# Kernel tuning notes

Hardware: AMD Instinct MI355X
Metric: run time of the kernel (lower is better)

The kernel has to match this reference:

```python
import jax, jax.numpy as jnp
import numpy as np

N, D_IN, D, E, B = 30000, 512, 512, 300000, 4096
N_RES, N_DNN = 2, 2
EPS = 1e-5


def _ln(x, g, b):
    mu = jnp.mean(x, axis=-1, keepdims=True)
    var = jnp.mean((x - mu) ** 2, axis=-1, keepdims=True)
    return (x - mu) * jax.lax.rsqrt(var + EPS) * g + b


def setup_inputs() -> dict:
    key = jax.random.key(0)
    ks = jax.random.split(key, 16)
    s = 1.0 / np.sqrt(D)
    inp = {
        "node_feat": jax.random.normal(ks[0], (N, D_IN), jnp.float32),
        "edge_hop0": jax.random.randint(ks[1], (2, E), 0, N, jnp.int32),
        "edge_hop1": jax.random.randint(ks[2], (2, E), 0, N, jnp.int32),
        "target_idx": jax.random.randint(ks[3], (B,), 0, N, jnp.int32),
        # node transform
        "Wt": jax.random.normal(ks[4], (D_IN, D), jnp.float32) / np.sqrt(D_IN),
        "bt": jnp.zeros((D,), jnp.float32),
        # GATConv (shared across both hops, one relation)
        "Wf": jax.random.normal(ks[5], (D, D), jnp.float32) * s,
        "bf": jnp.zeros((D,), jnp.float32),
        "w_att": jax.random.normal(ks[6], (2 * D,), jnp.float32) * s,
        "b_att": jnp.zeros((), jnp.float32),
        "gat_bias": jnp.zeros((D,), jnp.float32),
        # Res_DNN
        "Wp": jax.random.normal(ks[7], (D, D), jnp.float32) * s,
        "bp": jnp.zeros((D,), jnp.float32),
        "dnn_W": jax.random.normal(ks[8], (N_RES, N_DNN, D, D), jnp.float32) * s,
        "dnn_b": jnp.zeros((N_RES, N_DNN, D), jnp.float32),
        "dnn_g": jnp.ones((N_RES, N_DNN, D), jnp.float32),
        "dnn_beta": jnp.zeros((N_RES, N_DNN, D), jnp.float32),
        "res_g": jnp.ones((N_RES, D), jnp.float32),
        "res_beta": jnp.zeros((N_RES, D), jnp.float32),
        "Wc": jax.random.normal(ks[9], (D, 1), jnp.float32) * s,
        "bc": jnp.zeros((1,), jnp.float32),
    }
    return inp


def _gat(feat, edges, Wf, bf, w_att, b_att, gat_bias):
    # dst and src are the same node set / same features here
    h = feat @ Wf + bf                      # [N, D]
    di, si = edges[0], edges[1]             # [E], [E]
    # att(concat(dst_h, src_h)) == dst_h @ w[:D] + src_h @ w[D:] + b
    sd = h @ w_att[:D]                      # [N]
    ss = h @ w_att[D:]                      # [N]
    e = jnp.tanh(sd[di] + ss[si] + b_att)   # [E]
    # sparse softmax per destination row
    m = jax.ops.segment_max(e, di, num_segments=N)
    a = jnp.exp(e - m[di])
    denom = jax.ops.segment_sum(a, di, num_segments=N)
    alpha = a / denom[di]                   # [E]
    # sparse-mm aggregation
    out = jax.ops.segment_sum(alpha[:, None] * h[si], di, num_segments=N)
    return out + gat_bias


def reference(node_feat, edge_hop0, edge_hop1, target_idx, Wt, bt, Wf, bf,
              w_att, b_att, gat_bias, Wp, bp, dnn_W, dnn_b, dnn_g, dnn_beta,
              res_g, res_beta, Wc, bc):
    # node-type feature transform (dropout is identity at inference)
    feat = node_feat @ Wt + bt              # [N, D]
    # hops processed from last to first: hop1 then hop0
    for edges in (edge_hop1, edge_hop0):
        g = _gat(feat, edges, Wf, bf, w_att, b_att, gat_bias)
        feat = (feat + g) * 0.5             # mean of stacked [orig, gat_out]
    h = feat[target_idx]                    # [B, D]
    # Res_DNN head
    h = h @ Wp + bp
    for r in range(N_RES):
        sc = h
        for i in range(N_DNN):
            h = _ln(jnp.tanh(h @ dnn_W[r, i] + dnn_b[r, i]), dnn_g[r, i], dnn_beta[r, i])
        h = _ln(jnp.tanh(sc + h), res_g[r], res_beta[r])
    logits = h @ Wc + bc                    # [B, 1]
    return jax.nn.sigmoid(logits)
```

## Files before the change

### kernel.cpp

```cpp
#include <hip/hip_runtime.h>

#define D 512
typedef unsigned short ushort_t;
typedef __attribute__((ext_vector_type(8))) short bf16x8;
typedef __attribute__((ext_vector_type(4))) float f32x4;

static __device__ __forceinline__ ushort_t f2bf(float f) {
  unsigned u = __float_as_uint(f);
  u += 0x7fffu + ((u >> 16) & 1u);
  return (ushort_t)(u >> 16);
}
static __device__ __forceinline__ float bf2f(ushort_t h) {
  return __uint_as_float(((unsigned)h) << 16);
}

static __device__ __forceinline__ void gld_lds16(const void* g, void* lds) {
  __builtin_amdgcn_global_load_lds(
      (const __attribute__((address_space(1))) unsigned int*)g,
      (__attribute__((address_space(3))) unsigned int*)lds, 16, 0, 0);
}

__global__ __launch_bounds__(256) void pack_weight7(
    const float* __restrict__ Wt, const float* __restrict__ Wf,
    const float* __restrict__ Wp, const float* __restrict__ Wd,
    ushort_t* __restrict__ out) {
  const int per = D * D;
  int i = blockIdx.x * 256 + threadIdx.x;
  if (i >= per * 7) return;
  const int mat = i / per;
  const int r = i - mat * per;
  const float* W;
  if (mat == 0) W = Wt;
  else if (mat == 1) W = Wf;
  else if (mat == 2) W = Wp;
  else W = Wd + (size_t)(mat - 3) * per;
  const int k = r / D, n = r - k * D;
  const int nt = n >> 4, col = n & 15, kt = k >> 5, kg = (k >> 3) & 3, j = k & 7;
  out[(size_t)mat * per + (((size_t)nt * (D >> 5) + kt) << 9) + ((kg << 4) + col) * 8 + j] =
      f2bf(W[r]);
}

__global__ __launch_bounds__(256) void conv_bf16_pad(
    const float* __restrict__ in, ushort_t* __restrict__ out, int M, int Mp, int K) {
  const size_t i4 = ((size_t)blockIdx.x * 256 + threadIdx.x) * 4;
  if (i4 >= (size_t)Mp * K) return;
  const int row = (int)(i4 / K);
  ushort4 o;
  if (row < M) {
    const float4 v = *reinterpret_cast<const float4*>(&in[i4]);
    o.x = f2bf(v.x); o.y = f2bf(v.y); o.z = f2bf(v.z); o.w = f2bf(v.w);
  } else {
    o.x = o.y = o.z = o.w = 0;
  }
  *reinterpret_cast<ushort4*>(&out[i4]) = o;
}

__global__ __launch_bounds__(256) void init_buffers(
    int* __restrict__ cnt, int* __restrict__ tflag, int* __restrict__ nflag,
    int* __restrict__ counters, int Nn, int N2) {
  const int i = blockIdx.x * 256 + threadIdx.x;
  if (i < N2) cnt[i] = 0;
  if (i < Nn) { tflag[i] = 0; nflag[i] = 0; }
  if (i < 2) counters[i * 64] = 0;
}

__global__ void fill_bucket(const int* __restrict__ e1, const int* __restrict__ e0,
                            const int* __restrict__ tidx, int* __restrict__ tflag,
                            int* __restrict__ cnt, int* __restrict__ bucket,
                            int Nn, int E, int B) {
  const int e = blockIdx.x * blockDim.x + threadIdx.x;
  if (e < B) tflag[tidx[e]] = 1;
  if (e >= E) return;
  const int d1 = e1[e];
  const int p1 = atomicAdd(&cnt[d1], 1);
  if (p1 < 64) bucket[(size_t)d1 * 64 + p1] = e1[E + e];
  const int d0 = e0[e];
  const int p0 = atomicAdd(&cnt[Nn + d0], 1);
  if (p0 < 64) bucket[((size_t)(Nn + d0)) * 64 + p0] = e0[E + e];
}

__global__ void flag_srcs(const int* __restrict__ e0, const int* __restrict__ tflag,
                          int* __restrict__ nflag, int E) {
  const int e = blockIdx.x * blockDim.x + threadIdx.x;
  if (e < E && tflag[e0[e]]) nflag[e0[E + e]] = 1;
}

__global__ void compact2(const int* __restrict__ tflag, const int* __restrict__ nflag,
                         int* __restrict__ tlist, int* __restrict__ nlist,
                         int* __restrict__ counters, int Nn) {
  const int i = blockIdx.x * 256 + threadIdx.x;
  if (i >= Nn) return;
  const int tf = tflag[i];
  if (tf) tlist[atomicAdd(&counters[0], 1)] = i;
  if (tf | nflag[i]) nlist[atomicAdd(&counters[64], 1)] = i;
}

__global__ __launch_bounds__(512) void gemm_mfma(
    const ushort_t* __restrict__ A, const ushort_t* __restrict__ Bp,
    const float* __restrict__ bias, ushort_t* __restrict__ C16,
    const float* __restrict__ watt, float* __restrict__ sd_part,
    float* __restrict__ ss_part, int Mp, int N, int K) {
  __shared__ __align__(16) ushort_t As[2][8 * 512];
  __shared__ __align__(16) ushort_t Bs[2][8 * 512];
  const int nwg = gridDim.x;
  const int q = nwg >> 3, rm = nwg & 7;
  const int xcd = blockIdx.x & 7, kk = blockIdx.x >> 3;
  const int lin = (xcd < rm ? xcd * (q + 1) : rm * (q + 1) + (xcd - rm) * q) + kk;
  const int m0 = (lin >> 2) * 128;
  const int n0 = (lin & 3) * 128;
  const int tid = threadIdx.x;
  const int lane = tid & 63;
  const int wid = tid >> 6;
  const int wm = wid >> 1;
  const int wn = wid & 1;
  const int arow = lane & 15;
  const int akoff = (lane >> 4) * 8;
  const int c15 = lane & 15;
  const int rgrp = lane >> 4;
  const int kt32 = K >> 5;
  f32x4 acc[2][4] = {};

  auto stage = [&](int kt, int b) {
    const int k0 = kt * 32;
    gld_lds16(&A[(size_t)(m0 + wid * 16 + arow) * K + k0 + akoff],
              &As[b][wid * 512]);
    gld_lds16(&Bp[(((size_t)(n0 / 16 + wid) * kt32 + kt) << 9) + lane * 8],
              &Bs[b][wid * 512]);
  };

  stage(0, 0);
  __syncthreads();
  int cur = 0;
  for (int t = 0; t < kt32; ++t) {
    if (t + 1 < kt32) stage(t + 1, cur ^ 1);
    bf16x8 af[2], bfr[4];
#pragma unroll
    for (int mi = 0; mi < 2; ++mi)
      af[mi] = *reinterpret_cast<const bf16x8*>(&As[cur][(wm * 2 + mi) * 512 + lane * 8]);
#pragma unroll
    for (int ni = 0; ni < 4; ++ni)
      bfr[ni] = *reinterpret_cast<const bf16x8*>(&Bs[cur][(wn * 4 + ni) * 512 + lane * 8]);
#pragma unroll
    for (int mi = 0; mi < 2; ++mi)
#pragma unroll
      for (int ni = 0; ni < 4; ++ni)
        acc[mi][ni] = __builtin_amdgcn_mfma_f32_16x16x32_bf16(af[mi], bfr[ni], acc[mi][ni], 0, 0, 0);
    __syncthreads();
    cur ^= 1;
  }
  const int band = (n0 >> 6) + wn;
#pragma unroll
  for (int mi = 0; mi < 2; ++mi) {
    const int row = m0 + wm * 32 + mi * 16 + (rgrp << 2);
#pragma unroll
    for (int r = 0; r < 4; ++r) {
      float psd = 0.f, pss = 0.f;
#pragma unroll
      for (int ni = 0; ni < 4; ++ni) {
        const int col = n0 + wn * 64 + ni * 16 + c15;
        const float v = acc[mi][ni][r] + bias[col];
        C16[(size_t)(row + r) * N + col] = f2bf(v);
        if (watt) {
          psd += v * watt[col];
          pss += v * watt[D + col];
        }
      }
      if (watt) {
#pragma unroll
        for (int off = 8; off > 0; off >>= 1) {
          psd += __shfl_xor(psd, off);
          pss += __shfl_xor(pss, off);
        }
        if (c15 == 0) {
          sd_part[(size_t)band * Mp + row + r] = psd;
          ss_part[(size_t)band * Mp + row + r] = pss;
        }
      }
    }
  }
}

__global__ __launch_bounds__(256) void combine_dots(
    const float* __restrict__ sd_part, const float* __restrict__ ss_part,
    float* __restrict__ sd, float* __restrict__ ss, int Mp, int Nn) {
  const int i = blockIdx.x * 256 + threadIdx.x;
  if (i >= Nn) return;
  float a = 0.f, b = 0.f;
#pragma unroll
  for (int bnd = 0; bnd < 8; ++bnd) {
    a += sd_part[(size_t)bnd * Mp + i];
    b += ss_part[(size_t)bnd * Mp + i];
  }
  sd[i] = a;
  ss[i] = b;
}

__global__ __launch_bounds__(256) void gat_aggregate_w(
    ushort_t* __restrict__ featb, const ushort_t* __restrict__ hb,
    const float* __restrict__ sd, const float* __restrict__ ss,
    const int* __restrict__ di, const int* __restrict__ si,
    const float* __restrict__ b_att_p, const float* __restrict__ gat_bias,
    const int* __restrict__ cnt, const int* __restrict__ bucket,
    const int* __restrict__ dstlist, const int* __restrict__ dcount,
    int Nn, int E) {
  const int gidx = blockIdx.x * 4 + (threadIdx.x >> 6);
  const int lane = threadIdx.x & 63;
  if (gidx >= *dcount) return;
  const int dst = dstlist[gidx];
  const int deg = cnt[dst];
  const float sdd = sd[dst];
  const float ba = b_att_p[0];
  const size_t o = (size_t)dst * D + lane * 8;
  bf16x8 fv = *reinterpret_cast<const bf16x8*>(&featb[o]);
  float acc[8] = {};
  if (deg <= 64) {
    const bool valid = lane < deg;
    const int slane = valid ? bucket[(size_t)dst * 64 + lane] : 0;
    const float e = valid ? tanhf(sdd + ss[slane] + ba) : -1e30f;
    float m = e;
#pragma unroll
    for (int off = 32; off > 0; off >>= 1) m = fmaxf(m, __shfl_xor(m, off));
    const float a = valid ? expf(e - m) : 0.f;
    float s = a;
#pragma unroll
    for (int off = 32; off > 0; off >>= 1) s += __shfl_xor(s, off);
    const float w = a * ((s > 0.f) ? 1.f / s : 0.f);
    int k = 0;
    for (; k + 3 < deg; k += 4) {
      const float w0 = __shfl(w, k), w1 = __shfl(w, k + 1);
      const float w2 = __shfl(w, k + 2), w3 = __shfl(w, k + 3);
      const int s0 = __shfl(slane, k), s1 = __shfl(slane, k + 1);
      const int s2 = __shfl(slane, k + 2), s3 = __shfl(slane, k + 3);
      const bf16x8 h0 = *reinterpret_cast<const bf16x8*>(&hb[(size_t)s0 * D + lane * 8]);
      const bf16x8 h1 = *reinterpret_cast<const bf16x8*>(&hb[(size_t)s1 * D + lane * 8]);
      const bf16x8 h2 = *reinterpret_cast<const bf16x8*>(&hb[(size_t)s2 * D + lane * 8]);
      const bf16x8 h3 = *reinterpret_cast<const bf16x8*>(&hb[(size_t)s3 * D + lane * 8]);
#pragma unroll
      for (int qq = 0; qq < 8; ++qq) {
        const float t0 = w0 * bf2f((ushort_t)h0[qq]) + w1 * bf2f((ushort_t)h1[qq]);
        const float t1 = w2 * bf2f((ushort_t)h2[qq]) + w3 * bf2f((ushort_t)h3[qq]);
        acc[qq] += t0 + t1;
      }
    }
    for (; k < deg; ++k) {
      const float wk = __shfl(w, k);
      const int sk = __shfl(slane, k);
      const bf16x8 h0 = *reinterpret_cast<const bf16x8*>(&hb[(size_t)sk * D + lane * 8]);
#pragma unroll
      for (int qq = 0; qq < 8; ++qq) acc[qq] += wk * bf2f((ushort_t)h0[qq]);
    }
  } else {
    float m = -1e30f;
    for (int e = lane; e < E; e += 64)
      if (di[e] == dst) m = fmaxf(m, tanhf(sdd + ss[si[e]] + ba));
#pragma unroll
    for (int off = 32; off > 0; off >>= 1) m = fmaxf(m, __shfl_xor(m, off));
    float s = 0.f;
    for (int e = lane; e < E; e += 64)
      if (di[e] == dst) s += expf(tanhf(sdd + ss[si[e]] + ba) - m);
#pragma unroll
    for (int off = 32; off > 0; off >>= 1) s += __shfl_xor(s, off);
    const float inv = (s > 0.f) ? 1.f / s : 0.f;
    for (int base = 0; base < E; base += 64) {
      const int e = base + lane;
      const bool hit = (e < E) && (di[e] == dst);
      unsigned long long mask = __ballot(hit);
      const int sidx = hit ? si[e] : 0;
      const float aval = hit ? expf(tanhf(sdd + ss[sidx] + ba) - m) * inv : 0.f;
      while (mask) {
        const int l = __ffsll((long long)mask) - 1;
        mask &= mask - 1;
        const float wv = __shfl(aval, l);
        const int sk = __shfl(sidx, l);
        const bf16x8 hv = *reinterpret_cast<const bf16x8*>(&hb[(size_t)sk * D + lane * 8]);
#pragma unroll
        for (int qq = 0; qq < 8; ++qq) acc[qq] += wv * bf2f((ushort_t)hv[qq]);
      }
    }
  }
#pragma unroll
  for (int q = 0; q < 8; ++q) {
    const float f = (bf2f((ushort_t)fv[q]) + acc[q] + gat_bias[lane * 8 + q]) * 0.5f;
    fv[q] = (short)f2bf(f);
  }
  *reinterpret_cast<bf16x8*>(&featb[o]) = fv;
}

__global__ __launch_bounds__(1024, 4) void head_fused(
    const ushort_t* __restrict__ featb, const int* __restrict__ tidx,
    const ushort_t* __restrict__ pWp, const float* __restrict__ bp,
    const ushort_t* __restrict__ pDW, const float* __restrict__ dnn_b,
    const float* __restrict__ dnn_g, const float* __restrict__ dnn_be,
    const float* __restrict__ res_g, const float* __restrict__ res_be,
    const float* __restrict__ Wc, const float* __restrict__ bc,
    float* __restrict__ out) {
  __shared__ __align__(16) ushort_t A_lds[16 * 512];
  __shared__ float lsum[16][16], lsq[16][16], meanv[16], rsv[16];
  const int tid = threadIdx.x;
  const int lane = tid & 63;
  const int wave = tid >> 6;
  const int nt0 = wave * 2;
  const int c15 = lane & 15;
  const int rgrp = lane >> 4;

  {
    const int row = tid >> 6, col8 = tid & 63;
    const int g = tidx[blockIdx.x * 16 + row];
    const bf16x8 v = *reinterpret_cast<const bf16x8*>(&featb[(size_t)g * D + col8 * 8]);
    *reinterpret_cast<bf16x8*>(&A_lds[row * 512 + (col8 ^ (row & 7)) * 8]) = v;
  }
  __syncthreads();

  auto do_gemm = [&](const ushort_t* __restrict__ W, f32x4& a0, f32x4& a1) {
    a0 = f32x4{0.f, 0.f, 0.f, 0.f};
    a1 = f32x4{0.f, 0.f, 0.f, 0.f};
    bf16x8 c0[4], c1[4];
#pragma unroll
    for (int d = 0; d < 4; ++d) {
      c0[d] = *reinterpret_cast<const bf16x8*>(
          &W[(((size_t)nt0 * 16 + d) << 9) + lane * 8]);
      c1[d] = *reinterpret_cast<const bf16x8*>(
          &W[(((size_t)(nt0 + 1) * 16 + d) << 9) + lane * 8]);
    }
#pragma unroll
    for (int kt = 0; kt < 16; ++kt) {
      const int slot = kt & 3;
      const bf16x8 w0 = c0[slot];
      const bf16x8 w1 = c1[slot];
      if (kt + 4 < 16) {
        c0[slot] = *reinterpret_cast<const bf16x8*>(
            &W[(((size_t)nt0 * 16 + kt + 4) << 9) + lane * 8]);
        c1[slot] = *reinterpret_cast<const bf16x8*>(
            &W[(((size_t)(nt0 + 1) * 16 + kt + 4) << 9) + lane * 8]);
      }
      const int col8 = kt * 4 + rgrp;
      const bf16x8 af = *reinterpret_cast<const bf16x8*>(
          &A_lds[c15 * 512 + (col8 ^ (c15 & 7)) * 8]);
      a0 = __builtin_amdgcn_mfma_f32_16x16x32_bf16(af, w0, a0, 0, 0, 0);
      a1 = __builtin_amdgcn_mfma_f32_16x16x32_bf16(af, w1, a1, 0, 0, 0);
    }
  };

  auto block_ln = [&](f32x4& v0, f32x4& v1, const float* __restrict__ g,
                      const float* __restrict__ be) {
    float psum[4], psq[4];
#pragma unroll
    for (int r = 0; r < 4; ++r) {
      psum[r] = v0[r] + v1[r];
      psq[r] = v0[r] * v0[r] + v1[r] * v1[r];
    }
#pragma unroll
    for (int off = 8; off > 0; off >>= 1)
#pragma unroll
      for (int r = 0; r < 4; ++r) {
        psum[r] += __shfl_xor(psum[r], off);
        psq[r] += __shfl_xor(psq[r], off);
      }
    if (c15 == 0) {
#pragma unroll
      for (int r = 0; r < 4; ++r) {
        lsum[wave][rgrp * 4 + r] = psum[r];
        lsq[wave][rgrp * 4 + r] = psq[r];
      }
    }
    __syncthreads();
    if (tid < 16) {
      float s = 0.f, qq = 0.f;
#pragma unroll
      for (int w = 0; w < 16; ++w) { s += lsum[w][tid]; qq += lsq[w][tid]; }
      const float mean = s * (1.f / 512.f);
      const float var = qq * (1.f / 512.f) - mean * mean;
      meanv[tid] = mean;
      rsv[tid] = rsqrtf(var + 1e-5f);
    }
    __syncthreads();
    const int col0 = nt0 * 16 + c15;
    const int col1 = (nt0 + 1) * 16 + c15;
    const float g0 = g[col0], b0 = be[col0];
    const float g1 = g[col1], b1 = be[col1];
#pragma unroll
    for (int r = 0; r < 4; ++r) {
      const int row = rgrp * 4 + r;
      v0[r] = (v0[r] - meanv[row]) * rsv[row] * g0 + b0;
      v1[r] = (v1[r] - meanv[row]) * rsv[row] * g1 + b1;
    }
  };

  auto store_A = [&](const f32x4& v0, const f32x4& v1) {
    const int col0 = nt0 * 16 + c15;
    const int col1 = (nt0 + 1) * 16 + c15;
#pragma unroll
    for (int r = 0; r < 4; ++r) {
      const int row = rgrp * 4 + r;
      A_lds[row * 512 + (((col0 >> 3) ^ (row & 7)) << 3) + (col0 & 7)] = f2bf(v0[r]);
      A_lds[row * 512 + (((col1 >> 3) ^ (row & 7)) << 3) + (col1 & 7)] = f2bf(v1[r]);
    }
  };

  f32x4 sc0, sc1, acc0, acc1, ln0, ln1;

  do_gemm(pWp, acc0, acc1);
  {
    const float bv0 = bp[nt0 * 16 + c15];
    const float bv1 = bp[(nt0 + 1) * 16 + c15];
#pragma unroll
    for (int r = 0; r < 4; ++r) { sc0[r] = acc0[r] + bv0; sc1[r] = acc1[r] + bv1; }
  }
  __syncthreads();
  store_A(sc0, sc1);
  __syncthreads();

  for (int rb = 0; rb < 2; ++rb) {
    {
      const int st = rb * 2;
      do_gemm(pDW + (size_t)st * D * D, acc0, acc1);
      const float bv0 = dnn_b[st * D + nt0 * 16 + c15];
      const float bv1 = dnn_b[st * D + (nt0 + 1) * 16 + c15];
#pragma unroll
      for (int r = 0; r < 4; ++r) {
        acc0[r] = tanhf(acc0[r] + bv0);
        acc1[r] = tanhf(acc1[r] + bv1);
      }
      block_ln(acc0, acc1, dnn_g + st * D, dnn_be + st * D);
      store_A(acc0, acc1);
      __syncthreads();
    }
    {
      const int st = rb * 2 + 1;
      do_gemm(pDW + (size_t)st * D * D, ln0, ln1);
      const float bv0 = dnn_b[st * D + nt0 * 16 + c15];
      const float bv1 = dnn_b[st * D + (nt0 + 1) * 16 + c15];
#pragma unroll
      for (int r = 0; r < 4; ++r) {
        ln0[r] = tanhf(ln0[r] + bv0);
        ln1[r] = tanhf(ln1[r] + bv1);
      }
      block_ln(ln0, ln1, dnn_g + st * D, dnn_be + st * D);
    }
#pragma unroll
    for (int r = 0; r < 4; ++r) {
      acc0[r] = tanhf(sc0[r] + ln0[r]);
      acc1[r] = tanhf(sc1[r] + ln1[r]);
    }
    block_ln(acc0, acc1, res_g + rb * D, res_be + rb * D);
    sc0 = acc0;
    sc1 = acc1;
    if (rb == 0) {
      store_A(sc0, sc1);
      __syncthreads();
    }
  }

  float pr[4];
  {
    const float w0 = Wc[nt0 * 16 + c15];
    const float w1 = Wc[(nt0 + 1) * 16 + c15];
#pragma unroll
    for (int r = 0; r < 4; ++r) pr[r] = sc0[r] * w0 + sc1[r] * w1;
  }
#pragma unroll
  for (int off = 8; off > 0; off >>= 1)
#pragma unroll
    for (int r = 0; r < 4; ++r) pr[r] += __shfl_xor(pr[r], off);
  __syncthreads();
  if (c15 == 0) {
#pragma unroll
    for (int r = 0; r < 4; ++r) lsum[wave][rgrp * 4 + r] = pr[r];
  }
  __syncthreads();
  if (tid < 16) {
    float s = 0.f;
#pragma unroll
    for (int w = 0; w < 16; ++w) s += lsum[w][tid];
    out[blockIdx.x * 16 + tid] = 1.f / (1.f + expf(-(s + bc[0])));
  }
}

extern "C" void kernel_launch(void* const* d_in, const int* in_sizes, int n_in,
                              void* d_out, int out_size, void* d_ws, size_t ws_size,
                              hipStream_t stream) {
  (void)n_in; (void)out_size; (void)ws_size;
  const float* node_feat = (const float*)d_in[0];
  const int* edge0 = (const int*)d_in[1];
  const int* edge1 = (const int*)d_in[2];
  const int* tidx = (const int*)d_in[3];
  const float* Wt = (const float*)d_in[4];
  const float* bt = (const float*)d_in[5];
  const float* Wf = (const float*)d_in[6];
  const float* bfp = (const float*)d_in[7];
  const float* w_att = (const float*)d_in[8];
  const float* b_att = (const float*)d_in[9];
  const float* gat_bias = (const float*)d_in[10];
  const float* Wp = (const float*)d_in[11];
  const float* bp = (const float*)d_in[12];
  const float* dnn_W = (const float*)d_in[13];
  const float* dnn_b = (const float*)d_in[14];
  const float* dnn_g = (const float*)d_in[15];
  const float* dnn_be = (const float*)d_in[16];
  const float* res_g = (const float*)d_in[17];
  const float* res_be = (const float*)d_in[18];
  const float* Wc = (const float*)d_in[19];
  const float* bc = (const float*)d_in[20];
  float* out = (float*)d_out;

  const int Nn = in_sizes[0] / D;
  const int E = in_sizes[1] / 2;
  const int B = in_sizes[3];
  const int K_IN = in_sizes[4] / D;
  const int Mp = (Nn + 127) / 128 * 128;
  const int N2 = 2 * Nn;

  char* p = (char*)d_ws;
  auto alloc = [&](size_t bytes) -> char* {
    char* r = p;
    p += (bytes + 255) & ~(size_t)255;
    return r;
  };
  ushort_t* featb = (ushort_t*)alloc((size_t)Mp * D * 2);
  ushort_t* hb = (ushort_t*)alloc((size_t)Mp * D * 2);
  float* sd = (float*)alloc((size_t)Nn * 4);
  float* ss = (float*)alloc((size_t)Nn * 4);
  float* sd_part = (float*)alloc((size_t)8 * Mp * 4);
  float* ss_part = (float*)alloc((size_t)8 * Mp * 4);
  int* cnt = (int*)alloc((size_t)N2 * 4);
  int* bucket = (int*)alloc((size_t)N2 * 64 * 4);
  int* tflag = (int*)alloc((size_t)Nn * 4);
  int* nflag = (int*)alloc((size_t)Nn * 4);
  int* tlist = (int*)alloc((size_t)B * 4);
  int* nlist = (int*)alloc((size_t)Nn * 4);
  int* counters = (int*)alloc(512);
  ushort_t* pAll = (ushort_t*)alloc((size_t)7 * D * D * 2);
  ushort_t* pWt = pAll;
  ushort_t* pWf = pAll + (size_t)D * D;
  ushort_t* pWp = pAll + (size_t)2 * D * D;
  ushort_t* pDWall = pAll + (size_t)3 * D * D;

  dim3 blk(256);

  pack_weight7<<<(7 * D * D + 255) / 256, blk, 0, stream>>>(Wt, Wf, Wp, dnn_W, pAll);
  conv_bf16_pad<<<((size_t)Mp * K_IN / 4 + 255) / 256, blk, 0, stream>>>(
      node_feat, hb , Nn, Mp, K_IN);

  init_buffers<<<(N2 + 255) / 256, blk, 0, stream>>>(cnt, tflag, nflag, counters, Nn, N2);
  fill_bucket<<<(E + 255) / 256, blk, 0, stream>>>(edge1, edge0, tidx, tflag,
                                                   cnt, bucket, Nn, E, B);
  flag_srcs<<<(E + 255) / 256, blk, 0, stream>>>(edge0, tflag, nflag, E);
  compact2<<<(Nn + 255) / 256, blk, 0, stream>>>(tflag, nflag, tlist, nlist,
                                                 counters, Nn);

  gemm_mfma<<<dim3(4 * (Mp / 128)), dim3(512), 0, stream>>>(
      hb, pWt, bt, featb, nullptr, nullptr, nullptr, Mp, D, K_IN);

  const int* hops[2] = {edge1, edge0};
  for (int hp = 0; hp < 2; ++hp) {
    gemm_mfma<<<dim3(4 * (Mp / 128)), dim3(512), 0, stream>>>(
        featb, pWf, bfp, hb, w_att, sd_part, ss_part, Mp, D, D);
    combine_dots<<<(Nn + 255) / 256, blk, 0, stream>>>(sd_part, ss_part, sd, ss, Mp, Nn);
    if (hp == 0) {
      gat_aggregate_w<<<(Nn + 3) / 4, blk, 0, stream>>>(
          featb, hb, sd, ss, hops[hp], hops[hp] + E, b_att, gat_bias,
          cnt + hp * Nn, bucket + (size_t)hp * Nn * 64, nlist, &counters[64], Nn, E);
    } else {
      gat_aggregate_w<<<(B + 3) / 4, blk, 0, stream>>>(
          featb, hb, sd, ss, hops[hp], hops[hp] + E, b_att, gat_bias,
          cnt + hp * Nn, bucket + (size_t)hp * Nn * 64, tlist, &counters[0], Nn, E);
    }
  }

  head_fused<<<B / 16, dim3(1024), 0, stream>>>(
      featb, tidx, pWp, bp, pDWall, dnn_b, dnn_g, dnn_be, res_g, res_be,
      Wc, bc, out);
}
```

Measured before the change: 294.0 us.

## Shrink head_fused to 8 rows per block with 512 threads, 4 N-tiles per wave

The fused MLP head now handles 8 target rows per block instead of 16, using 8 waves that each own 4 output column tiles. Rows 8-15 of the 16-row MFMA operand are zero-padded, and the grid doubles to B/8 blocks. The explicit 4-deep register prefetch of weight fragments is removed in favour of direct loads inside the k loop. This spreads the head across more blocks to raise CU coverage, at the cost of half the MFMA work being spent on padding rows and each block re-reading the full weight matrices.

```diff
diff --git a/kernel.cpp b/kernel.cpp
--- a/kernel.cpp
+++ b/kernel.cpp
@@ -286,7 +286,7 @@
   *reinterpret_cast<bf16x8*>(&featb[o]) = fv;
 }
 
-__global__ __launch_bounds__(1024, 4) void head_fused(
+__global__ __launch_bounds__(512, 4) void head_fused(
     const ushort_t* __restrict__ featb, const int* __restrict__ tidx,
     const ushort_t* __restrict__ pWp, const float* __restrict__ bp,
     const ushort_t* __restrict__ pDW, const float* __restrict__ dnn_b,
@@ -295,60 +295,53 @@
     const float* __restrict__ Wc, const float* __restrict__ bc,
     float* __restrict__ out) {
   __shared__ __align__(16) ushort_t A_lds[16 * 512];
-  __shared__ float lsum[16][16], lsq[16][16], meanv[16], rsv[16];
+  __shared__ float lsum[8][8], lsq[8][8], meanv[8], rsv[8];
   const int tid = threadIdx.x;
   const int lane = tid & 63;
   const int wave = tid >> 6;
-  const int nt0 = wave * 2;
+  const int nt0 = wave * 4;
   const int c15 = lane & 15;
   const int rgrp = lane >> 4;
 
   {
     const int row = tid >> 6, col8 = tid & 63;
-    const int g = tidx[blockIdx.x * 16 + row];
+    const int g = tidx[blockIdx.x * 8 + row];
     const bf16x8 v = *reinterpret_cast<const bf16x8*>(&featb[(size_t)g * D + col8 * 8]);
     *reinterpret_cast<bf16x8*>(&A_lds[row * 512 + (col8 ^ (row & 7)) * 8]) = v;
+    const int rz = row + 8;
+    *reinterpret_cast<bf16x8*>(&A_lds[rz * 512 + (col8 ^ (rz & 7)) * 8]) = bf16x8{};
   }
   __syncthreads();
 
-  auto do_gemm = [&](const ushort_t* __restrict__ W, f32x4& a0, f32x4& a1) {
-    a0 = f32x4{0.f, 0.f, 0.f, 0.f};
-    a1 = f32x4{0.f, 0.f, 0.f, 0.f};
-    bf16x8 c0[4], c1[4];
-#pragma unroll
-    for (int d = 0; d < 4; ++d) {
-      c0[d] = *reinterpret_cast<const bf16x8*>(
-          &W[(((size_t)nt0 * 16 + d) << 9) + lane * 8]);
-      c1[d] = *reinterpret_cast<const bf16x8*>(
-          &W[(((size_t)(nt0 + 1) * 16 + d) << 9) + lane * 8]);
-    }
+  auto do_gemm = [&](const ushort_t* __restrict__ W, f32x4* a) {
+#pragma unroll
+    for (int ni = 0; ni < 4; ++ni) a[ni] = f32x4{0.f, 0.f, 0.f, 0.f};
 #pragma unroll
     for (int kt = 0; kt < 16; ++kt) {
-      const int slot = kt & 3;
-      const bf16x8 w0 = c0[slot];
-      const bf16x8 w1 = c1[slot];
-      if (kt + 4 < 16) {
-        c0[slot] = *reinterpret_cast<const bf16x8*>(
-            &W[(((size_t)nt0 * 16 + kt + 4) << 9) + lane * 8]);
-        c1[slot] = *reinterpret_cast<const bf16x8*>(
-            &W[(((size_t)(nt0 + 1) * 16 + kt + 4) << 9) + lane * 8]);
-      }
       const int col8 = kt * 4 + rgrp;
       const bf16x8 af = *reinterpret_cast<const bf16x8*>(
           &A_lds[c15 * 512 + (col8 ^ (c15 & 7)) * 8]);
-      a0 = __builtin_amdgcn_mfma_f32_16x16x32_bf16(af, w0, a0, 0, 0, 0);
-      a1 = __builtin_amdgcn_mfma_f32_16x16x32_bf16(af, w1, a1, 0, 0, 0);
+#pragma unroll
+      for (int ni = 0; ni < 4; ++ni) {
+        const bf16x8 w = *reinterpret_cast<const bf16x8*>(
+            &W[(((size_t)(nt0 + ni) * 16 + kt) << 9) + lane * 8]);
+        a[ni] = __builtin_amdgcn_mfma_f32_16x16x32_bf16(af, w, a[ni], 0, 0, 0);
+      }
     }
   };
 
-  auto block_ln = [&](f32x4& v0, f32x4& v1, const float* __restrict__ g,
+  auto block_ln = [&](f32x4* v, const float* __restrict__ g,
                       const float* __restrict__ be) {
     float psum[4], psq[4];
 #pragma unroll
-    for (int r = 0; r < 4; ++r) {
-      psum[r] = v0[r] + v1[r];
-      psq[r] = v0[r] * v0[r] + v1[r] * v1[r];
-    }
+    for (int r = 0; r < 4; ++r) { psum[r] = 0.f; psq[r] = 0.f; }
+#pragma unroll
+    for (int ni = 0; ni < 4; ++ni)
+#pragma unroll
+      for (int r = 0; r < 4; ++r) {
+        psum[r] += v[ni][r];
+        psq[r] += v[ni][r] * v[ni][r];
+      }
 #pragma unroll
     for (int off = 8; off > 0; off >>= 1)
 #pragma unroll
@@ -356,7 +349,7 @@
         psum[r] += __shfl_xor(psum[r], off);
         psq[r] += __shfl_xor(psq[r], off);
       }
-    if (c15 == 0) {
+    if (c15 == 0 && rgrp < 2) {
 #pragma unroll
       for (int r = 0; r < 4; ++r) {
         lsum[wave][rgrp * 4 + r] = psum[r];
@@ -364,115 +357,116 @@
       }
     }
     __syncthreads();
-    if (tid < 16) {
+    if (tid < 8) {
       float s = 0.f, qq = 0.f;
 #pragma unroll
-      for (int w = 0; w < 16; ++w) { s += lsum[w][tid]; qq += lsq[w][tid]; }
+      for (int w = 0; w < 8; ++w) { s += lsum[w][tid]; qq += lsq[w][tid]; }
       const float mean = s * (1.f / 512.f);
       const float var = qq * (1.f / 512.f) - mean * mean;
       meanv[tid] = mean;
       rsv[tid] = rsqrtf(var + 1e-5f);
     }
     __syncthreads();
-    const int col0 = nt0 * 16 + c15;
-    const int col1 = (nt0 + 1) * 16 + c15;
-    const float g0 = g[col0], b0 = be[col0];
-    const float g1 = g[col1], b1 = be[col1];
-#pragma unroll
-    for (int r = 0; r < 4; ++r) {
-      const int row = rgrp * 4 + r;
-      v0[r] = (v0[r] - meanv[row]) * rsv[row] * g0 + b0;
-      v1[r] = (v1[r] - meanv[row]) * rsv[row] * g1 + b1;
+#pragma unroll
+    for (int ni = 0; ni < 4; ++ni) {
+      const int col = (nt0 + ni) * 16 + c15;
+      const float gg = g[col], bb = be[col];
+#pragma unroll
+      for (int r = 0; r < 4; ++r) {
+        const int row = (rgrp * 4 + r) & 7;
+        v[ni][r] = (v[ni][r] - meanv[row]) * rsv[row] * gg + bb;
+      }
     }
   };
 
-  auto store_A = [&](const f32x4& v0, const f32x4& v1) {
-    const int col0 = nt0 * 16 + c15;
-    const int col1 = (nt0 + 1) * 16 + c15;
-#pragma unroll
-    for (int r = 0; r < 4; ++r) {
-      const int row = rgrp * 4 + r;
-      A_lds[row * 512 + (((col0 >> 3) ^ (row & 7)) << 3) + (col0 & 7)] = f2bf(v0[r]);
-      A_lds[row * 512 + (((col1 >> 3) ^ (row & 7)) << 3) + (col1 & 7)] = f2bf(v1[r]);
+  auto store_A = [&](const f32x4* v) {
+    if (rgrp >= 2) return;
+#pragma unroll
+    for (int ni = 0; ni < 4; ++ni) {
+      const int col = (nt0 + ni) * 16 + c15;
+#pragma unroll
+      for (int r = 0; r < 4; ++r) {
+        const int row = rgrp * 4 + r;
+        A_lds[row * 512 + (((col >> 3) ^ (row & 7)) << 3) + (col & 7)] = f2bf(v[ni][r]);
+      }
     }
   };
 
-  f32x4 sc0, sc1, acc0, acc1, ln0, ln1;
-
-  do_gemm(pWp, acc0, acc1);
-  {
-    const float bv0 = bp[nt0 * 16 + c15];
-    const float bv1 = bp[(nt0 + 1) * 16 + c15];
-#pragma unroll
-    for (int r = 0; r < 4; ++r) { sc0[r] = acc0[r] + bv0; sc1[r] = acc1[r] + bv1; }
+  f32x4 sc[4], acc[4], ln[4];
+
+  do_gemm(pWp, acc);
+#pragma unroll
+  for (int ni = 0; ni < 4; ++ni) {
+    const float bv = bp[(nt0 + ni) * 16 + c15];
+#pragma unroll
+    for (int r = 0; r < 4; ++r) sc[ni][r] = acc[ni][r] + bv;
   }
   __syncthreads();
-  store_A(sc0, sc1);
+  store_A(sc);
   __syncthreads();
 
   for (int rb = 0; rb < 2; ++rb) {
     {
       const int st = rb * 2;
-      do_gemm(pDW + (size_t)st * D * D, acc0, acc1);
-      const float bv0 = dnn_b[st * D + nt0 * 16 + c15];
-      const float bv1 = dnn_b[st * D + (nt0 + 1) * 16 + c15];
-#pragma unroll
-      for (int r = 0; r < 4; ++r) {
-        acc0[r] = tanhf(acc0[r] + bv0);
-        acc1[r] = tanhf(acc1[r] + bv1);
-      }
-      block_ln(acc0, acc1, dnn_g + st * D, dnn_be + st * D);
-      store_A(acc0, acc1);
+      do_gemm(pDW + (size_t)st * D * D, acc);
+#pragma unroll
+      for (int ni = 0; ni < 4; ++ni) {
+        const float bv = dnn_b[st * D + (nt0 + ni) * 16 + c15];
+#pragma unroll
+        for (int r = 0; r < 4; ++r) acc[ni][r] = tanhf(acc[ni][r] + bv);
+      }
+      block_ln(acc, dnn_g + st * D, dnn_be + st * D);
+      store_A(acc);
       __syncthreads();
     }
     {
       const int st = rb * 2 + 1;
-      do_gemm(pDW + (size_t)st * D * D, ln0, ln1);
-      const float bv0 = dnn_b[st * D + nt0 * 16 + c15];
-      const float bv1 = dnn_b[st * D + (nt0 + 1) * 16 + c15];
-#pragma unroll
-      for (int r = 0; r < 4; ++r) {
-        ln0[r] = tanhf(ln0[r] + bv0);
-        ln1[r] = tanhf(ln1[r] + bv1);
-      }
-      block_ln(ln0, ln1, dnn_g + st * D, dnn_be + st * D);
-    }
-#pragma unroll
-    for (int r = 0; r < 4; ++r) {
-      acc0[r] = tanhf(sc0[r] + ln0[r]);
-      acc1[r] = tanhf(sc1[r] + ln1[r]);
-    }
-    block_ln(acc0, acc1, res_g + rb * D, res_be + rb * D);
-    sc0 = acc0;
-    sc1 = acc1;
+      do_gemm(pDW + (size_t)st * D * D, ln);
+#pragma unroll
+      for (int ni = 0; ni < 4; ++ni) {
+        const float bv = dnn_b[st * D + (nt0 + ni) * 16 + c15];
+#pragma unroll
+        for (int r = 0; r < 4; ++r) ln[ni][r] = tanhf(ln[ni][r] + bv);
+      }
+      block_ln(ln, dnn_g + st * D, dnn_be + st * D);
+    }
+#pragma unroll
+    for (int ni = 0; ni < 4; ++ni)
+#pragma unroll
+      for (int r = 0; r < 4; ++r) acc[ni][r] = tanhf(sc[ni][r] + ln[ni][r]);
+    block_ln(acc, res_g + rb * D, res_be + rb * D);
+#pragma unroll
+    for (int ni = 0; ni < 4; ++ni) sc[ni] = acc[ni];
     if (rb == 0) {
-      store_A(sc0, sc1);
+      store_A(sc);
       __syncthreads();
     }
   }
 
   float pr[4];
-  {
-    const float w0 = Wc[nt0 * 16 + c15];
-    const float w1 = Wc[(nt0 + 1) * 16 + c15];
-#pragma unroll
-    for (int r = 0; r < 4; ++r) pr[r] = sc0[r] * w0 + sc1[r] * w1;
+#pragma unroll
+  for (int r = 0; r < 4; ++r) pr[r] = 0.f;
+#pragma unroll
+  for (int ni = 0; ni < 4; ++ni) {
+    const float wv = Wc[(nt0 + ni) * 16 + c15];
+#pragma unroll
+    for (int r = 0; r < 4; ++r) pr[r] += sc[ni][r] * wv;
   }
 #pragma unroll
   for (int off = 8; off > 0; off >>= 1)
 #pragma unroll
     for (int r = 0; r < 4; ++r) pr[r] += __shfl_xor(pr[r], off);
   __syncthreads();
-  if (c15 == 0) {
+  if (c15 == 0 && rgrp < 2) {
 #pragma unroll
     for (int r = 0; r < 4; ++r) lsum[wave][rgrp * 4 + r] = pr[r];
   }
   __syncthreads();
-  if (tid < 16) {
+  if (tid < 8) {
     float s = 0.f;
 #pragma unroll
-    for (int w = 0; w < 16; ++w) s += lsum[w][tid];
-    out[blockIdx.x * 16 + tid] = 1.f / (1.f + expf(-(s + bc[0])));
+    for (int w = 0; w < 8; ++w) s += lsum[w][tid];
+    out[blockIdx.x * 8 + tid] = 1.f / (1.f + expf(-(s + bc[0])));
   }
 }
 
@@ -567,7 +561,7 @@
     }
   }
 
-  head_fused<<<B / 16, dim3(1024), 0, stream>>>(
+  head_fused<<<B / 8, dim3(512), 0, stream>>>(
       featb, tidx, pWp, bp, pDWall, dnn_b, dnn_g, dnn_be, res_g, res_be,
       Wc, bc, out);
 }
```

After: 339.2 us. 1.15x slower.
